# Performance work log

Hardware: AMD Instinct MI355X
Metric: run time of the kernel (lower is better)

The kernel has to match this reference:

```python
import jax, jax.numpy as jnp
import numpy as np

N_EXPERTS, D_MODEL, D_FF = 8, 1024, 2048
N_TOKENS, TOP_K = 4 * 2048, 2


def setup_inputs() -> dict:
    key = jax.random.key(0)
    ks = jax.random.split(key, 6)
    std = (1.0 / 3.0) ** 0.5
    return {
        "x": jax.random.normal(ks[0], (4, 2048, D_MODEL), dtype=jnp.float32),
        "expert_indices": jax.random.randint(ks[1], (N_TOKENS, TOP_K), 0, N_EXPERTS, dtype=jnp.int64),
        "expert_weights": jax.random.uniform(ks[2], (N_TOKENS, TOP_K), dtype=jnp.float32),
        "w1": jax.random.normal(ks[3], (N_EXPERTS, D_MODEL, D_FF), dtype=jnp.float32) * (std / D_MODEL ** 0.5),
        "w2": jax.random.normal(ks[4], (N_EXPERTS, D_MODEL, D_FF), dtype=jnp.float32) * (std / D_MODEL ** 0.5),
        "w3": jax.random.normal(ks[5], (N_EXPERTS, D_FF, D_MODEL), dtype=jnp.float32) * (std / D_FF ** 0.5),
    }


def reference(x, expert_indices, expert_weights, w1, w2, w3):
    input_shape = x.shape
    d = x.shape[-1]
    xt = x.reshape(-1, d)                      # [N, d_model]
    n_tokens = xt.shape[0]
    n_experts = w1.shape[0]
    # Dense routing matrix [N, E]: sum of top-k weights per (token, expert).
    # Equivalent to the original's per-pair scatter (index_add) combine.
    route = jnp.zeros((n_tokens, n_experts), dtype=xt.dtype)
    route = route.at[jnp.arange(n_tokens)[:, None], expert_indices].add(expert_weights)

    def step(acc, ws):
        w1e, w2e, w3e, re = ws
        hidden = jax.nn.silu(xt @ w1e) * (xt @ w2e)   # SwiGLU [N, d_ff]
        return acc + re[:, None] * (hidden @ w3e), None

    out, _ = jax.lax.scan(step, jnp.zeros_like(xt), (w1, w2, w3, route.T))
    return out.reshape(input_shape)
```

## Files before the change

### kernel.cpp

```cpp
#include <hip/hip_runtime.h>
#include <cstdint>

typedef unsigned short u16;
typedef u16 u16x8 __attribute__((ext_vector_type(8)));
typedef __bf16 bf16x8 __attribute__((ext_vector_type(8)));
typedef float f32x4 __attribute__((ext_vector_type(4)));

#define DEV static __device__ __forceinline__

constexpr int NT = 8192;
constexpr int NP = NT * 2;
constexpr int NE = 8;
constexpr int DM = 1024;
constexpr int DF = 2048;
constexpr int MAXS = 17664;
constexpr int MAXT128 = 136;
constexpr int NWG1 = 8 * 142;
constexpr int NWG2 = 8 * MAXT128;
constexpr int NTRANS = 24 * 512;
constexpr int NPREP = MAXS + NTRANS;

DEV u16 f2bf(float f) {
  uint32_t u = __builtin_bit_cast(uint32_t, f);
  u += 0x7fffu + ((u >> 16) & 1u);
  return (u16)(u >> 16);
}

DEV float bflo(uint32_t u) { return __builtin_bit_cast(float, u << 16); }
DEV float bfhi(uint32_t u) { return __builtin_bit_cast(float, u & 0xffff0000u); }

DEV void gload16(const void* g, void* l) {
  __builtin_amdgcn_global_load_lds((const __attribute__((address_space(1))) void*)g,
                                   (__attribute__((address_space(3))) void*)l, 16, 0, 0);
}

DEV bf16x8 ldfrag(const char* p) { return __builtin_bit_cast(bf16x8, *(const u16x8*)p); }

DEV f32x4 MFMA(bf16x8 a, bf16x8 b, f32x4 c) {
  return __builtin_amdgcn_mfma_f32_16x16x32_bf16(a, b, c, 0, 0, 0);
}

__global__ void k_route(const int* __restrict__ eidx, const float* __restrict__ ew,
                        int* meta, int* slot_token, float* slot_weight, int* pair_slot) {
  __shared__ int cnt[NE], cur[NE], off[NE];
  const int tid = threadIdx.x;
  if (tid < NE) { cnt[tid] = 0; cur[tid] = 0; }
  __syncthreads();
  for (int p = tid; p < NP; p += 1024) atomicAdd(&cnt[eidx[p] & 7], 1);
  __syncthreads();
  if (tid == 0) {
    int o = 0, t2 = 0, t1 = 0;
    for (int e = 0; e < NE; ++e) {
      off[e] = o; meta[e] = cnt[e]; meta[16 + e] = o;
      const int c = cnt[e];
      o += ((c + 127) >> 7) << 7;
      for (int mt = 0; mt * 256 < c; ++mt) meta[32 + t2++] = e | (mt << 8);
      for (int mt = 0; mt * 128 < c; ++mt) meta[128 + t1++] = e | (mt << 8);
    }
    meta[24] = o; meta[25] = t2; meta[26] = t1;
  }
  __syncthreads();
  for (int s = tid; s < MAXS; s += 1024) slot_token[s] = -1;
  __syncthreads();
  for (int p = tid; p < NP; p += 1024) {
    const int e = eidx[p] & 7;
    const int pos = off[e] + atomicAdd(&cur[e], 1);
    slot_token[pos]  = p >> 1;
    slot_weight[pos] = ew[p];
    pair_slot[p] = pos;
  }
}

__global__ void k_prep(const float* __restrict__ x, const int* __restrict__ slot_token,
                       u16* __restrict__ Xg,
                       const float* __restrict__ w1, const float* __restrict__ w2,
                       const float* __restrict__ w3, u16* __restrict__ w1T,
                       u16* __restrict__ w2T, u16* __restrict__ w3T) {
  __shared__ u16 tile[64][72];
  const int bid = blockIdx.x;
  const int t = threadIdx.x;

  if (bid < MAXS) {
    const int tok = slot_token[bid];
    const int c = t * 4;
    alignas(8) u16 b[4] = {0, 0, 0, 0};
    if (tok >= 0) {
      const float4 v = *reinterpret_cast<const float4*>(x + (size_t)tok * DM + c);
      b[0] = f2bf(v.x); b[1] = f2bf(v.y); b[2] = f2bf(v.z); b[3] = f2bf(v.w);
    }
    *reinterpret_cast<uint2*>(Xg + (size_t)bid * DM + c) = *reinterpret_cast<const uint2*>(b);
    return;
  }

  const int fid = bid - MAXS;
  const int z = fid >> 9;
  const int id = fid & 511;
  const int which = z >> 3, e = z & 7;
  const float* s; u16* d; int K, N, n0, k0;
  const size_t mo = (size_t)e * DM * DF;
  if (which == 0)      { s = w1 + mo; d = w1T + mo; K = DM; N = DF; n0 = (id & 31) * 64; k0 = (id >> 5) * 64; }
  else if (which == 1) { s = w2 + mo; d = w2T + mo; K = DM; N = DF; n0 = (id & 31) * 64; k0 = (id >> 5) * 64; }
  else                 { s = w3 + mo; d = w3T + mo; K = DF; N = DM; n0 = (id & 15) * 64; k0 = (id >> 4) * 64; }

  const int r = t >> 4, cb = (t & 15) * 4;
#pragma unroll
  for (int it = 0; it < 4; ++it) {
    const float4 v = *reinterpret_cast<const float4*>(s + (size_t)(k0 + r + it * 16) * N + n0 + cb);
    tile[r + it * 16][cb + 0] = f2bf(v.x);
    tile[r + it * 16][cb + 1] = f2bf(v.y);
    tile[r + it * 16][cb + 2] = f2bf(v.z);
    tile[r + it * 16][cb + 3] = f2bf(v.w);
  }
  __syncthreads();
  const int nl = t >> 2, ks = (t & 3) * 16;
  alignas(16) u16 vals[16];
#pragma unroll
  for (int j = 0; j < 16; ++j) vals[j] = tile[ks + j][nl];
  u16* dp = d + (size_t)(n0 + nl) * K + k0 + ks;
  *reinterpret_cast<uint4*>(dp)     = *reinterpret_cast<const uint4*>(vals);
  *reinterpret_cast<uint4*>(dp + 8) = *reinterpret_cast<const uint4*>(vals + 8);
}

__global__ __launch_bounds__(512, 2)
void k_gemm1(const u16* __restrict__ Xg, const u16* __restrict__ w1T, const u16* __restrict__ w2T,
             u16* __restrict__ H, const int* __restrict__ meta) {
  const int bid = blockIdx.x;
  const int xcd = bid & 7;
  const int local = bid >> 3;
  const int ti = local >> 1;
  if (ti >= meta[25]) return;
  const int n0 = (xcd * 2 + (local & 1)) * 128;
  const int ent = meta[32 + ti];
  const int e = ent & 255, mt = ent >> 8;
  const int base = meta[16 + e];
  const int cntp = meta[17 + e] - base;

  __shared__ __align__(16) char sm[2][65536];

  const int tid = threadIdx.x;
  const int lane = tid & 63;
  const int w = tid >> 6;
  const int wr = w >> 2, wc = w & 3;
  const int lrow = lane & 15, lk = lane >> 4;
  const int SX = lrow & 7;
  int cofs[2];
  cofs[0] = ((0 * 4 + lk) ^ SX) * 16;
  cofs[1] = ((1 * 4 + lk) ^ SX) * 16;
  const int Abase  = (wr * 128 + lrow) * 128;
  const int B1base = 32768 + (wc * 32 + lrow) * 128;
  const int B2base = B1base + 16384;

  const int srow8 = tid >> 3;
  const int scolw = ((tid & 7) ^ (srow8 & 7)) * 16;

  const char* AgT = (const char*)(Xg + (size_t)(base + mt * 256) * DM) + (size_t)srow8 * 2048 + scolw;
  const char* B1T = (const char*)(w1T + ((size_t)e * DF + n0) * DM)    + (size_t)srow8 * 2048 + scolw;
  const char* B2T = (const char*)(w2T + ((size_t)e * DF + n0) * DM)    + (size_t)srow8 * 2048 + scolw;

  f32x4 acc1[8][2] = {};
  f32x4 acc2[8][2] = {};

  auto SP = [&](char* d, size_t kb, int q) {
    switch (q) {
      case 0: gload16(AgT + kb,          d + tid * 16);
              gload16(AgT + 131072 + kb, d + 8192  + tid * 16); break;
      case 1: gload16(AgT + 262144 + kb, d + 16384 + tid * 16);
              gload16(AgT + 393216 + kb, d + 24576 + tid * 16); break;
      case 2: gload16(B1T + kb,          d + 32768 + tid * 16);
              gload16(B1T + 131072 + kb, d + 40960 + tid * 16); break;
      case 3: gload16(B2T + kb,          d + 49152 + tid * 16);
              gload16(B2T + 131072 + kb, d + 57344 + tid * 16); break;
    }
  };

  bf16x8 b1f[2][2], b2f[2][2];

  auto LDA4 = [&](const char* s, int mh, int ks, bf16x8* a) {
#pragma unroll
    for (int j = 0; j < 4; ++j)
      a[j] = ldfrag(s + Abase + mh * 8192 + j * 2048 + cofs[ks]);
  };
  auto MF16 = [&](int mh, int ks, const bf16x8* a) {
    __builtin_amdgcn_s_setprio(1);
#pragma unroll
    for (int j = 0; j < 4; ++j)
#pragma unroll
      for (int n = 0; n < 2; ++n) {
        acc1[mh * 4 + j][n] = MFMA(a[j], b1f[n][ks], acc1[mh * 4 + j][n]);
        acc2[mh * 4 + j][n] = MFMA(a[j], b2f[n][ks], acc2[mh * 4 + j][n]);
      }
    __builtin_amdgcn_s_setprio(0);
  };

  SP(sm[0], 0, 0); SP(sm[0], 0, 1); SP(sm[0], 0, 2); SP(sm[0], 0, 3);

  for (int kt = 0; kt < 16; ++kt) {
    const char* s = sm[kt & 1];
    char* d = sm[(kt + 1) & 1];
    const size_t kbn = (size_t)((kt + 1 < 16) ? kt + 1 : 15) * 128;
    bf16x8 a[4];

    SP(d, kbn, 0);
    asm volatile("s_waitcnt vmcnt(2)" ::: "memory");
    __builtin_amdgcn_s_barrier();
#pragma unroll
    for (int n = 0; n < 2; ++n)
#pragma unroll
      for (int s2 = 0; s2 < 2; ++s2) {
        b1f[n][s2] = ldfrag(s + B1base + n * 2048 + cofs[s2]);
        b2f[n][s2] = ldfrag(s + B2base + n * 2048 + cofs[s2]);
      }
    LDA4(s, 0, 0, a);
    MF16(0, 0, a);
    __builtin_amdgcn_s_barrier();

    LDA4(s, 1, 0, a);
    SP(d, kbn, 1);
    __builtin_amdgcn_s_barrier();
    MF16(1, 0, a);
    __builtin_amdgcn_s_barrier();

    LDA4(s, 0, 1, a);
    SP(d, kbn, 2);
    __builtin_amdgcn_s_barrier();
    MF16(0, 1, a);
    __builtin_amdgcn_s_barrier();

    LDA4(s, 1, 1, a);
    SP(d, kbn, 3);
    __builtin_amdgcn_s_barrier();
    MF16(1, 1, a);
    __builtin_amdgcn_s_barrier();
  }

  u16* Hrow = H + (size_t)(base + mt * 256) * DF + n0;
#pragma unroll
  for (int m = 0; m < 8; ++m)
#pragma unroll
    for (int r = 0; r < 4; ++r) {
      const int rloc = wr * 128 + m * 16 + lk * 4 + r;
      if (mt * 256 + rloc >= cntp) continue;
      u16* hp = Hrow + (size_t)rloc * DF + wc * 32 + lrow;
#pragma unroll
      for (int n = 0; n < 2; ++n) {
        const float h1 = acc1[m][n][r], h2 = acc2[m][n][r];
        const float sv = h1 / (1.f + __expf(-h1)) * h2;
        hp[n * 16] = f2bf(sv);
      }
    }
}

__global__ __launch_bounds__(256, 2)
void k_gemm2(const u16* __restrict__ H, const u16* __restrict__ w3T, const int* __restrict__ meta,
             const float* __restrict__ slot_weight, u16* __restrict__ O) {
  const int bid = blockIdx.x;
  const int ti = bid >> 3;
  if (ti >= meta[26]) return;
  const int n0 = (bid & 7) * 128;
  const int ent = meta[128 + ti];
  const int e = ent & 255, mt = ent >> 8;
  const int base = meta[16 + e];

  __shared__ __align__(16) char sm[2][32768];

  const int tid = threadIdx.x;
  const int lane = tid & 63;
  const int w = tid >> 6;
  const int wr = w >> 1, wc = w & 1;
  const int lrow = lane & 15, lk = lane >> 4;
  const int SX = lrow & 7;
  int cofs[2];
  cofs[0] = ((0 * 4 + lk) ^ SX) * 16;
  cofs[1] = ((1 * 4 + lk) ^ SX) * 16;
  const int Abase = (wr * 64 + lrow) * 128;
  const int Bbase = 16384 + (wc * 64 + lrow) * 128;

  const int srow = tid >> 3;
  const int scolw = ((tid & 7) ^ (srow & 7)) * 16;

  const char* AgT = (const char*)(H + (size_t)(base + mt * 128) * DF) + (size_t)srow * 4096 + scolw;
  const char* BgT = (const char*)(w3T + ((size_t)e * DM + n0) * DF)   + (size_t)srow * 4096 + scolw;

  f32x4 acc[4][4] = {};

  auto SPA = [&](char* d, size_t kb) {
#pragma unroll
    for (int c = 0; c < 4; ++c)
      gload16(AgT + (size_t)c * 131072 + kb, d + c * 4096 + tid * 16);
  };
  auto SPB = [&](char* d, size_t kb) {
#pragma unroll
    for (int c = 0; c < 4; ++c)
      gload16(BgT + (size_t)c * 131072 + kb, d + 16384 + c * 4096 + tid * 16);
  };

  bf16x8 bf[4][2];

  auto LDA4 = [&](const char* s, int ks, bf16x8* a) {
#pragma unroll
    for (int j = 0; j < 4; ++j)
      a[j] = ldfrag(s + Abase + j * 2048 + cofs[ks]);
  };
  auto MF16 = [&](int ks, const bf16x8* a) {
    __builtin_amdgcn_s_setprio(1);
#pragma unroll
    for (int j = 0; j < 4; ++j)
#pragma unroll
      for (int n = 0; n < 4; ++n)
        acc[j][n] = MFMA(a[j], bf[n][ks], acc[j][n]);
    __builtin_amdgcn_s_setprio(0);
  };

  SPA(sm[0], 0); SPB(sm[0], 0);

  for (int kt = 0; kt < 32; ++kt) {
    const char* s = sm[kt & 1];
    char* d = sm[(kt + 1) & 1];
    const size_t kbn = (size_t)((kt + 1 < 32) ? kt + 1 : 31) * 128;
    bf16x8 a[4];

    SPA(d, kbn);
    asm volatile("s_waitcnt vmcnt(4)" ::: "memory");
    __builtin_amdgcn_s_barrier();
#pragma unroll
    for (int n = 0; n < 4; ++n)
#pragma unroll
      for (int s2 = 0; s2 < 2; ++s2)
        bf[n][s2] = ldfrag(s + Bbase + n * 2048 + cofs[s2]);
    LDA4(s, 0, a);
    MF16(0, a);
    __builtin_amdgcn_s_barrier();

    LDA4(s, 1, a);
    SPB(d, kbn);
    __builtin_amdgcn_s_barrier();
    MF16(1, a);
    __builtin_amdgcn_s_barrier();
  }

  const int sb = base + mt * 128;
#pragma unroll
  for (int m = 0; m < 4; ++m)
#pragma unroll
    for (int r = 0; r < 4; ++r) {
      const int rloc = wr * 64 + m * 16 + lk * 4 + r;
      const float wgt = slot_weight[sb + rloc];
      u16* op = O + (size_t)(sb + rloc) * DM + n0 + wc * 64 + lrow;
#pragma unroll
      for (int n = 0; n < 4; ++n)
        op[n * 16] = f2bf(wgt * acc[m][n][r]);
    }
}

__global__ void k_combine(const u16* __restrict__ O, const int* __restrict__ pair_slot,
                          float* __restrict__ out) {
  const int tok = blockIdx.x * 2 + (threadIdx.x >> 7);
  const int c = (threadIdx.x & 127) * 8;
  const int sa = pair_slot[2 * tok], sb = pair_slot[2 * tok + 1];
  const uint4 va = *reinterpret_cast<const uint4*>(O + (size_t)sa * DM + c);
  const uint4 vb = *reinterpret_cast<const uint4*>(O + (size_t)sb * DM + c);
  float4 r0, r1;
  r0.x = bflo(va.x) + bflo(vb.x);  r0.y = bfhi(va.x) + bfhi(vb.x);
  r0.z = bflo(va.y) + bflo(vb.y);  r0.w = bfhi(va.y) + bfhi(vb.y);
  r1.x = bflo(va.z) + bflo(vb.z);  r1.y = bfhi(va.z) + bfhi(vb.z);
  r1.z = bflo(va.w) + bflo(vb.w);  r1.w = bfhi(va.w) + bfhi(vb.w);
  float* op = out + (size_t)tok * DM + c;
  *reinterpret_cast<float4*>(op)     = r0;
  *reinterpret_cast<float4*>(op + 4) = r1;
}

extern "C" void kernel_launch(void* const* d_in, const int* in_sizes, int n_in,
                              void* d_out, int out_size, void* d_ws, size_t ws_size,
                              hipStream_t stream) {
  const float* x  = (const float*)d_in[0];
  const int* eidx = (const int*)d_in[1];
  const float* ew = (const float*)d_in[2];
  const float* w1 = (const float*)d_in[3];
  const float* w2 = (const float*)d_in[4];
  const float* w3 = (const float*)d_in[5];
  float* out = (float*)d_out;
  char* ws = (char*)d_ws;

  int* meta          = (int*)ws;
  int* pair_slot     = (int*)(ws + 2048);
  int* slot_token    = (int*)(ws + 2048 + 65536);
  float* slot_weight = (float*)(ws + 2048 + 65536 + (size_t)MAXS * 4);
  size_t off = 2048 + 65536 + (size_t)MAXS * 8;
  u16* Xg  = (u16*)(ws + off); off += (size_t)MAXS * DM * 2;
  u16* w1T = (u16*)(ws + off); off += (size_t)NE * DM * DF * 2;
  u16* w2T = (u16*)(ws + off); off += (size_t)NE * DM * DF * 2;
  u16* w3T = (u16*)(ws + off); off += (size_t)NE * DM * DF * 2;
  u16* H   = (u16*)(ws + off);
  u16* O   = Xg;

  k_route<<<1, 1024, 0, stream>>>(eidx, ew, meta, slot_token, slot_weight, pair_slot);
  k_prep<<<NPREP, 256, 0, stream>>>(x, slot_token, Xg, w1, w2, w3, w1T, w2T, w3T);
  k_gemm1<<<NWG1, 512, 0, stream>>>(Xg, w1T, w2T, H, meta);
  k_gemm2<<<NWG2, 256, 0, stream>>>(H, w3T, meta, slot_weight, O);
  k_combine<<<NT / 2, 256, 0, stream>>>(O, pair_slot, out);
}
```

Measured before the change: 374.9 us.

## Use a four-stage K=32 LDS pipeline in the gate/up GEMM

The gate/up GEMM kernel switches from a double-buffered K=64 tile to a four-buffer ring of K=32 tiles, with three stages of global-to-LDS loads in flight. The many barriers inside each K step are replaced by a single wait-and-barrier per step. The XOR swizzle is dropped, since the 64-byte LDS row layout lets fragment reads stay contiguous. The aim is to hide more global memory latency and cut synchronisation cost, at the price of twice as many loop iterations, each with less MFMA work to overlap with loads.

New measurement: 400.0 us. +6.7%, slower.

```diff
diff --git a/kernel.cpp b/kernel.cpp
--- a/kernel.cpp
+++ b/kernel.cpp
@@ -135,101 +135,69 @@
   const int base = meta[16 + e];
   const int cntp = meta[17 + e] - base;
 
-  __shared__ __align__(16) char sm[2][65536];
+  __shared__ __align__(16) char sm[4][32768];
 
   const int tid = threadIdx.x;
   const int lane = tid & 63;
   const int w = tid >> 6;
   const int wr = w >> 2, wc = w & 3;
   const int lrow = lane & 15, lk = lane >> 4;
-  const int SX = lrow & 7;
-  int cofs[2];
-  cofs[0] = ((0 * 4 + lk) ^ SX) * 16;
-  cofs[1] = ((1 * 4 + lk) ^ SX) * 16;
-  const int Abase  = (wr * 128 + lrow) * 128;
-  const int B1base = 32768 + (wc * 32 + lrow) * 128;
-  const int B2base = B1base + 16384;
-
-  const int srow8 = tid >> 3;
-  const int scolw = ((tid & 7) ^ (srow8 & 7)) * 16;
-
-  const char* AgT = (const char*)(Xg + (size_t)(base + mt * 256) * DM) + (size_t)srow8 * 2048 + scolw;
-  const char* B1T = (const char*)(w1T + ((size_t)e * DF + n0) * DM)    + (size_t)srow8 * 2048 + scolw;
-  const char* B2T = (const char*)(w2T + ((size_t)e * DF + n0) * DM)    + (size_t)srow8 * 2048 + scolw;
+  const int Abase  = (wr * 128 + lrow) * 64 + lk * 16;
+  const int B1base = 16384 + (wc * 32 + lrow) * 64 + lk * 16;
+  const int B2base = B1base + 8192;
+
+  const char* AgT = (const char*)(Xg + (size_t)(base + mt * 256) * DM) + (size_t)(tid >> 2) * 2048 + (tid & 3) * 16;
+  const char* B1T = (const char*)(w1T + ((size_t)e * DF + n0) * DM)    + (size_t)(tid >> 2) * 2048 + (tid & 3) * 16;
+  const char* B2T = (const char*)(w2T + ((size_t)e * DF + n0) * DM)    + (size_t)(tid >> 2) * 2048 + (tid & 3) * 16;
 
   f32x4 acc1[8][2] = {};
   f32x4 acc2[8][2] = {};
 
-  auto SP = [&](char* d, size_t kb, int q) {
-    switch (q) {
-      case 0: gload16(AgT + kb,          d + tid * 16);
-              gload16(AgT + 131072 + kb, d + 8192  + tid * 16); break;
-      case 1: gload16(AgT + 262144 + kb, d + 16384 + tid * 16);
-              gload16(AgT + 393216 + kb, d + 24576 + tid * 16); break;
-      case 2: gload16(B1T + kb,          d + 32768 + tid * 16);
-              gload16(B1T + 131072 + kb, d + 40960 + tid * 16); break;
-      case 3: gload16(B2T + kb,          d + 49152 + tid * 16);
-              gload16(B2T + 131072 + kb, d + 57344 + tid * 16); break;
-    }
-  };
-
-  bf16x8 b1f[2][2], b2f[2][2];
-
-  auto LDA4 = [&](const char* s, int mh, int ks, bf16x8* a) {
-#pragma unroll
-    for (int j = 0; j < 4; ++j)
-      a[j] = ldfrag(s + Abase + mh * 8192 + j * 2048 + cofs[ks]);
-  };
-  auto MF16 = [&](int mh, int ks, const bf16x8* a) {
+  auto STAGE = [&](char* d, int kt) {
+    const size_t kb = (size_t)kt * 64;
+    gload16(AgT + kb,          d + tid * 16);
+    gload16(AgT + 262144 + kb, d + 8192 + tid * 16);
+    gload16(B1T + kb,          d + 16384 + tid * 16);
+    gload16(B2T + kb,          d + 24576 + tid * 16);
+  };
+
+  auto MF16 = [&](int mbase, const bf16x8* a, const bf16x8* b1f, const bf16x8* b2f) {
     __builtin_amdgcn_s_setprio(1);
 #pragma unroll
     for (int j = 0; j < 4; ++j)
 #pragma unroll
       for (int n = 0; n < 2; ++n) {
-        acc1[mh * 4 + j][n] = MFMA(a[j], b1f[n][ks], acc1[mh * 4 + j][n]);
-        acc2[mh * 4 + j][n] = MFMA(a[j], b2f[n][ks], acc2[mh * 4 + j][n]);
+        acc1[mbase + j][n] = MFMA(a[j], b1f[n], acc1[mbase + j][n]);
+        acc2[mbase + j][n] = MFMA(a[j], b2f[n], acc2[mbase + j][n]);
       }
     __builtin_amdgcn_s_setprio(0);
   };
 
-  SP(sm[0], 0, 0); SP(sm[0], 0, 1); SP(sm[0], 0, 2); SP(sm[0], 0, 3);
-
-  for (int kt = 0; kt < 16; ++kt) {
-    const char* s = sm[kt & 1];
-    char* d = sm[(kt + 1) & 1];
-    const size_t kbn = (size_t)((kt + 1 < 16) ? kt + 1 : 15) * 128;
-    bf16x8 a[4];
-
-    SP(d, kbn, 0);
-    asm volatile("s_waitcnt vmcnt(2)" ::: "memory");
-    __builtin_amdgcn_s_barrier();
-#pragma unroll
-    for (int n = 0; n < 2; ++n)
-#pragma unroll
-      for (int s2 = 0; s2 < 2; ++s2) {
-        b1f[n][s2] = ldfrag(s + B1base + n * 2048 + cofs[s2]);
-        b2f[n][s2] = ldfrag(s + B2base + n * 2048 + cofs[s2]);
-      }
-    LDA4(s, 0, 0, a);
-    MF16(0, 0, a);
-    __builtin_amdgcn_s_barrier();
-
-    LDA4(s, 1, 0, a);
-    SP(d, kbn, 1);
-    __builtin_amdgcn_s_barrier();
-    MF16(1, 0, a);
-    __builtin_amdgcn_s_barrier();
-
-    LDA4(s, 0, 1, a);
-    SP(d, kbn, 2);
-    __builtin_amdgcn_s_barrier();
-    MF16(0, 1, a);
-    __builtin_amdgcn_s_barrier();
-
-    LDA4(s, 1, 1, a);
-    SP(d, kbn, 3);
-    __builtin_amdgcn_s_barrier();
-    MF16(1, 1, a);
+  STAGE(sm[0], 0); STAGE(sm[1], 1); STAGE(sm[2], 2);
+
+  for (int kt = 0; kt < 32; ++kt) {
+    const char* s = sm[kt & 3];
+    char* d = sm[(kt + 3) & 3];
+    const int kbn = (kt + 3 < 32) ? kt + 3 : 31;
+
+    STAGE(d, kbn);
+    asm volatile("s_waitcnt vmcnt(12)" ::: "memory");
+    __builtin_amdgcn_s_barrier();
+
+    bf16x8 b1f[2], b2f[2], a[4];
+#pragma unroll
+    for (int n = 0; n < 2; ++n) {
+      b1f[n] = ldfrag(s + B1base + n * 1024);
+      b2f[n] = ldfrag(s + B2base + n * 1024);
+    }
+#pragma unroll
+    for (int j = 0; j < 4; ++j)
+      a[j] = ldfrag(s + Abase + j * 1024);
+    MF16(0, a, b1f, b2f);
+#pragma unroll
+    for (int j = 0; j < 4; ++j)
+      a[j] = ldfrag(s + Abase + (4 + j) * 1024);
+    MF16(4, a, b1f, b2f);
     __builtin_amdgcn_s_barrier();
   }
 
```
